# Kernel tuning notes

Measured on AMD Instinct MI355X. Metric: run time of the kernel, lower is better.

## Reference

```python
import jax, jax.numpy as jnp
import numpy as np

EMB = 300
LAYERS = 5
N_NODES = 100000
N_EDGES = 400000
N_GRAPHS = 1024
TEMP = 0.04
BN_EPS = 1e-5
SELF_LOOP_BOND_TYPE = 4  # pretrain-gnns convention: self-loop edge_attr = [4, 0]


def setup_inputs() -> dict:
    key = jax.random.key(0)
    ks = jax.random.split(key, 20)
    s = 0.02
    inp = {
        "x": jax.random.randint(ks[0], (N_NODES, 2), 0, 3, dtype=jnp.int64) if jax.config.jax_enable_x64 else jax.random.randint(ks[0], (N_NODES, 2), 0, 3, dtype=jnp.int32),
        "edge_index": jax.random.randint(ks[1], (2, N_EDGES), 0, N_NODES, dtype=jnp.int32),
        "edge_attr": jax.random.randint(ks[2], (N_EDGES, 2), 0, 3, dtype=jnp.int32),
        "batch": jnp.sort(jax.random.randint(ks[3], (N_NODES,), 0, N_GRAPHS, dtype=jnp.int32)),
        # atom embedding tables
        "atom_emb1": jax.random.normal(ks[4], (120, EMB), jnp.float32) * s,
        "atom_emb2": jax.random.normal(ks[5], (3, EMB), jnp.float32) * s,
        # per-layer bond embedding tables
        "bond_emb1": jax.random.normal(ks[6], (LAYERS, 6, EMB), jnp.float32) * s,
        "bond_emb2": jax.random.normal(ks[7], (LAYERS, 3, EMB), jnp.float32) * s,
        # per-layer GIN MLP: Linear(300,600) -> ReLU -> Linear(600,300)
        "W1": jax.random.normal(ks[8], (LAYERS, EMB, 2 * EMB), jnp.float32) * s,
        "b1": jnp.zeros((LAYERS, 2 * EMB), jnp.float32),
        "W2": jax.random.normal(ks[9], (LAYERS, 2 * EMB, EMB), jnp.float32) * s,
        "b2": jnp.zeros((LAYERS, EMB), jnp.float32),
        # per-layer batchnorm affine params
        "bn_scale": jnp.ones((LAYERS, EMB), jnp.float32),
        "bn_bias": jnp.zeros((LAYERS, EMB), jnp.float32),
        # projector: Linear(300,300) -> ReLU -> Linear(300,300)
        "pW1": jax.random.normal(ks[10], (EMB, EMB), jnp.float32) * s,
        "pb1": jnp.zeros((EMB,), jnp.float32),
        "pW2": jax.random.normal(ks[11], (EMB, EMB), jnp.float32) * s,
        "pb2": jnp.zeros((EMB,), jnp.float32),
    }
    return inp


def _forward(x, edge_index, edge_attr, batch, atom_emb1, atom_emb2, bond_emb1,
             bond_emb2, W1, b1, W2, b2, bn_scale, bn_bias, pW1, pb1, pW2, pb2):
    src, dst = edge_index[0], edge_index[1]
    h = atom_emb1[x[:, 0]] + atom_emb2[x[:, 1]]  # [N, EMB]
    for l in range(LAYERS):
        # edge embeddings for real edges + self-loop edge embedding
        e_emb = bond_emb1[l][edge_attr[:, 0]] + bond_emb2[l][edge_attr[:, 1]]  # [E, EMB]
        self_emb = bond_emb1[l][SELF_LOOP_BOND_TYPE] + bond_emb2[l][0]  # [EMB]
        # GIN sum aggregation: scatter messages + implicit self-loop message
        msg = h[src] + e_emb  # [E, EMB]
        agg = jax.ops.segment_sum(msg, dst, num_segments=N_NODES) + h + self_emb
        # MLP
        h = jax.nn.relu(agg @ W1[l] + b1[l]) @ W2[l] + b2[l]
        # batchnorm (training-mode batch statistics)
        mean = jnp.mean(h, axis=0)
        var = jnp.var(h, axis=0)
        h = (h - mean) * jax.lax.rsqrt(var + BN_EPS) * bn_scale[l] + bn_bias[l]
        if l < LAYERS - 1:
            h = jax.nn.relu(h)
    # global mean pool over graphs
    counts = jax.ops.segment_sum(jnp.ones((N_NODES,), h.dtype), batch, num_segments=N_GRAPHS)
    pooled = jax.ops.segment_sum(h, batch, num_segments=N_GRAPHS) / jnp.maximum(counts, 1.0)[:, None]
    # projector + L2 normalize
    proj = jax.nn.relu(pooled @ pW1 + pb1) @ pW2 + pb2
    norm = jnp.sqrt(jnp.sum(proj * proj, axis=1, keepdims=True))
    feats = proj / jnp.maximum(norm, 1e-12)
    f0, f1 = feats[: N_GRAPHS // 2], feats[N_GRAPHS // 2:]
    logits = (f0 @ f1.T) / TEMP  # [G/2, G/2]
    return logits


def reference(x, edge_index, edge_attr, batch, atom_emb1, atom_emb2, bond_emb1,
              bond_emb2, W1, b1, W2, b2, bn_scale, bn_bias, pW1, pb1, pW2, pb2):
    return _forward(x, edge_index, edge_attr, batch, atom_emb1, atom_emb2,
                    bond_emb1, bond_emb2, W1, b1, W2, b2, bn_scale, bn_bias,
                    pW1, pb1, pW2, pb2)
```

## Files before the change

kernel.cpp:

```cpp
#include <hip/hip_runtime.h>

#define EMB   300
#define EMB2  600
#define NLAYERS 5
#define NN    100000
#define NE    400000
#define NG    1024
#define BN_EPS 1e-5f
#define MPAD  100096
#define NB_SC 391
#define HLD   304


typedef __bf16 bf16;
typedef __attribute__((ext_vector_type(4))) __bf16 bf16x4;
typedef __attribute__((ext_vector_type(8))) __bf16 bf16x8;
typedef __attribute__((ext_vector_type(4))) float f32x4;

typedef __attribute__((address_space(3))) unsigned int lds_uint;
typedef __attribute__((address_space(1))) const unsigned int gbl_uint;

__device__ __forceinline__ void gld_lds16(const bf16* g, bf16* l) {
  __builtin_amdgcn_global_load_lds((gbl_uint*)g, (lds_uint*)l, 16, 0, 0);
}

__global__ void k_count(const int* __restrict__ dst, int* __restrict__ cnt) {
  int e = blockIdx.x * 256 + threadIdx.x;
  if (e < NE) atomicAdd(&cnt[dst[e]], 1);
}

__global__ void k_bsum(const int* __restrict__ cnt, int* __restrict__ bsum) {
  __shared__ int red[256];
  int i = blockIdx.x * 256 + threadIdx.x;
  red[threadIdx.x] = (i < NN) ? cnt[i] : 0;
  __syncthreads();
  for (int off = 128; off; off >>= 1) {
    if (threadIdx.x < off) red[threadIdx.x] += red[threadIdx.x + off];
    __syncthreads();
  }
  if (!threadIdx.x) bsum[blockIdx.x] = red[0];
}

__global__ void k_bscan(const int* __restrict__ bsum, int* __restrict__ bpre) {
  __shared__ int s[512];
  int t = threadIdx.x;
  s[t] = (t < NB_SC) ? bsum[t] : 0;
  __syncthreads();
  for (int off = 1; off < 512; off <<= 1) {
    int v = (t >= off) ? s[t - off] : 0;
    __syncthreads();
    s[t] += v;
    __syncthreads();
  }
  if (t < NB_SC) bpre[t] = t ? s[t - 1] : 0;
}

__global__ void k_expand(const int* __restrict__ cnt, const int* __restrict__ bpre,
                         int* __restrict__ rowptr, int* __restrict__ cursor) {
  __shared__ int s[256];
  int t = threadIdx.x, i = blockIdx.x * 256 + t;
  int v = (i < NN) ? cnt[i] : 0;
  s[t] = v;
  __syncthreads();
  for (int off = 1; off < 256; off <<= 1) {
    int u = (t >= off) ? s[t - off] : 0;
    __syncthreads();
    s[t] += u;
    __syncthreads();
  }
  int excl = bpre[blockIdx.x] + s[t] - v;
  if (i < NN) { rowptr[i] = excl; cursor[i] = excl; }
  if (i == NN - 1) rowptr[NN] = excl + v;
}

__global__ void k_fill(const int* __restrict__ ei, const int* __restrict__ ea,
                       int* __restrict__ cursor, int* __restrict__ packed) {
  int e = blockIdx.x * 256 + threadIdx.x;
  if (e >= NE) return;
  int d = ei[NE + e];
  int s = ei[e];
  int comb = ea[2 * e] * 3 + ea[2 * e + 1];
  int pos = atomicAdd(&cursor[d], 1);
  packed[pos] = s | (comb << 20);
}

__global__ void k_init(const int* __restrict__ x, const float4* __restrict__ ae1,
                       const float4* __restrict__ ae2, bf16* __restrict__ h) {
  int idx = blockIdx.x * 256 + threadIdx.x;
  if (idx >= NN * 76) return;
  int n = idx / 76, v = idx - n * 76;
  bf16x4 r4;
  if (v < 75) {
    int x0 = x[2 * n], x1 = x[2 * n + 1];
    float4 a = ae1[x0 * 75 + v], b = ae2[x1 * 75 + v];
    r4[0] = (bf16)(a.x + b.x); r4[1] = (bf16)(a.y + b.y);
    r4[2] = (bf16)(a.z + b.z); r4[3] = (bf16)(a.w + b.w);
  } else {
    r4[0] = r4[1] = r4[2] = r4[3] = (bf16)0.f;
  }
  *(bf16x4*)(h + (size_t)n * HLD + 4 * v) = r4;
}

__global__ void k_prepw1(const float* __restrict__ W1, bf16* __restrict__ B1n) {
  int idx = blockIdx.x * 256 + threadIdx.x;
  if (idx >= 5 * 640 * 640) return;
  int l = idx / (640 * 640), rem = idx - l * (640 * 640);
  int n = rem / 640, kp = rem - n * 640;
  int lo = kp >= 320;
  int kk = lo ? kp - 320 : kp;
  float w = (n < 600 && kk < 300) ? W1[(size_t)l * 300 * 600 + kk * 600 + n] : 0.f;
  bf16 hi = (bf16)w;
  B1n[idx] = lo ? (bf16)(w - (float)hi) : hi;
}

__global__ void k_prepw2(const float* __restrict__ W2, bf16* __restrict__ B2n) {
  int idx = blockIdx.x * 256 + threadIdx.x;
  if (idx >= 5 * 384 * 1280) return;
  int l = idx / (384 * 1280), rem = idx - l * (384 * 1280);
  int n = rem / 1280, kp = rem - n * 1280;
  int lo = kp >= 640;
  int kk = lo ? kp - 640 : kp;
  float w = (n < 300 && kk < 600) ? W2[(size_t)l * 600 * 300 + kk * 300 + n] : 0.f;
  bf16 hi = (bf16)w;
  B2n[idx] = lo ? (bf16)(w - (float)hi) : hi;
}

__global__ void k_prepb(const float* __restrict__ b1, const float* __restrict__ b2,
                        float* __restrict__ b1p, float* __restrict__ b2p) {
  int idx = blockIdx.x * 256 + threadIdx.x;
  if (idx < 5 * 640) {
    int l = idx / 640, n = idx - l * 640;
    b1p[idx] = (n < 600) ? b1[l * 600 + n] : 0.f;
  } else if (idx < 5 * 640 + 5 * 384) {
    int j = idx - 5 * 640;
    int l = j / 384, n = j - l * 384;
    b2p[j] = (n < 300) ? b2[l * 300 + n] : 0.f;
  }
}

template <int APPLY>
__global__ __launch_bounds__(256) void k_agg(
    const bf16* __restrict__ h, const int* __restrict__ rowptr,
    const int* __restrict__ packed, const float* __restrict__ be1,
    const float* __restrict__ be2, const float* __restrict__ coef,
    bf16* __restrict__ aggS) {
  __shared__ float tab[9 * HLD];
  for (int i = threadIdx.x; i < 9 * HLD; i += 256) {
    int cc = i / HLD, d = i - cc * HLD;
    tab[i] = (d < EMB)
                 ? be1[(cc / 3) * EMB + d] + be2[(cc - (cc / 3) * 3) * EMB + d]
                 : 0.f;
  }
  __syncthreads();
  const int ty = threadIdx.x >> 6, lane = threadIdx.x & 63;
  const int n = blockIdx.x * 4 + ty;
  const int c = 8 * lane;
  const bool act = lane < 38;

  float a8[8], b8[8], acc[8];
  if (act) {
#pragma unroll
    for (int j = 0; j < 8; j++) {
      int d = c + j;
      a8[j] = APPLY ? coef[d] : 1.f;
      b8[j] = APPLY ? coef[HLD + d] : 0.f;
    }
    const bf16* hn = h + (size_t)n * HLD;
#pragma unroll
    for (int j = 0; j < 8; j++) {
      int d = c + j;
      float hv = (float)hn[d];
      if (APPLY) hv = fmaxf(fmaf(a8[j], hv, b8[j]), 0.f);
      acc[j] = hv + be1[4 * EMB + d] + be2[d];
    }
  }
  int e0 = rowptr[n], e1 = rowptr[n + 1];
  for (int e = e0; e < e1; ++e) {
    int pk = packed[e];
    const bf16* hr = h + (size_t)(pk & 0xFFFFF) * HLD;
    const float* tr = tab + (pk >> 20) * HLD;
    if (act) {
      bf16x8 v = *(const bf16x8*)(hr + c);
      f32x4 t0 = *(const f32x4*)(tr + c);
      f32x4 t1 = *(const f32x4*)(tr + c + 4);
#pragma unroll
      for (int j = 0; j < 8; j++) {
        float hv = (float)v[j];
        if (APPLY) hv = fmaxf(fmaf(a8[j], hv, b8[j]), 0.f);
        acc[j] += hv + (j < 4 ? t0[j] : t1[j - 4]);
      }
    }
  }
  bf16* row = aggS + (size_t)n * 320;
  if (lane < 40) {
    bf16x8 o;
#pragma unroll
    for (int j = 0; j < 8; j++)
      o[j] = (act && c + j < EMB) ? (bf16)acc[j] : (bf16)0.f;
    *(bf16x8*)(row + c) = o;
  }
}

template <int K_SECT, int LDA, int LDB, int B_LO, int MODE, int NTILE>
__global__ __launch_bounds__(512) void k_mfma(
    const bf16* __restrict__ A,
    const bf16* __restrict__ Bn,
    const float* __restrict__ bias,
    bf16* __restrict__ C, float* __restrict__ stats, int row_limit) {
  __shared__ __align__(16) bf16 As[256 * 64];
  __shared__ __align__(16) bf16 Bs0[128 * 64];
  __shared__ __align__(16) bf16 Bs1[128 * 64];
  const int t = threadIdx.x, lane = t & 63, wid = t >> 6;
  const int wr = wid >> 1, wc = wid & 1;

  const int nwg = (int)gridDim.x;
  const int q = nwg >> 3, r = nwg & 7;
  const int xcd = blockIdx.x & 7, slot = blockIdx.x >> 3;
  const int lin = (xcd < r ? xcd * (q + 1) : r * (q + 1) + (xcd - r) * q) + slot;
  const int row0 = (lin / NTILE) * 256, n0 = (lin % NTILE) * 128;

  const int csw = (lane & 7) ^ (lane >> 3);
  const int r8  = lane >> 3;

  auto stage = [&](int kt) {
    int kbase = kt * 64;
    const bf16* ga = A  + (size_t)(row0 + wid * 32 + r8) * LDA + kbase + csw * 8;
    const bf16* gb = Bn + (size_t)(n0  + wid * 16 + r8) * LDB + kbase + csw * 8;
#pragma unroll
    for (int i = 0; i < 4; i++)
      gld_lds16(ga + (size_t)(i * 8) * LDA, &As[(wid * 32 + i * 8) * 64]);
#pragma unroll
    for (int i = 0; i < 2; i++) {
      gld_lds16(gb + (size_t)(i * 8) * LDB,        &Bs0[(wid * 16 + i * 8) * 64]);
      gld_lds16(gb + (size_t)(i * 8) * LDB + B_LO, &Bs1[(wid * 16 + i * 8) * 64]);
    }
  };

  f32x4 acc[4][4] = {};
#pragma unroll 2
  for (int kt = 0; kt < K_SECT; kt++) {
    stage(kt);
    __syncthreads();
#pragma unroll
    for (int kk = 0; kk < 2; kk++) {
      bf16x8 af[4], b0[4], b1[4];
#pragma unroll
      for (int mf = 0; mf < 4; mf++) {
        int rr = wr * 64 + mf * 16 + (lane & 15);
        int c = (kk * 4 + (lane >> 4)) ^ (rr & 7);
        af[mf] = *(const bf16x8*)((const char*)&As[0] + rr * 128 + (c << 4));
      }
#pragma unroll
      for (int nf = 0; nf < 4; nf++) {
        int n = wc * 64 + nf * 16 + (lane & 15);
        int c = (kk * 4 + (lane >> 4)) ^ (n & 7);
        b0[nf] = *(const bf16x8*)((const char*)&Bs0[0] + n * 128 + (c << 4));
        b1[nf] = *(const bf16x8*)((const char*)&Bs1[0] + n * 128 + (c << 4));
      }
#pragma unroll
      for (int mf = 0; mf < 4; mf++)
#pragma unroll
        for (int nf = 0; nf < 4; nf++) {
          acc[mf][nf] = __builtin_amdgcn_mfma_f32_16x16x32_bf16(
              af[mf], b0[nf], acc[mf][nf], 0, 0, 0);
          acc[mf][nf] = __builtin_amdgcn_mfma_f32_16x16x32_bf16(
              af[mf], b1[nf], acc[mf][nf], 0, 0, 0);
        }
    }
    __syncthreads();
  }

  const int rq = (lane >> 4) << 2;
  const int cl = lane & 15;
#pragma unroll
  for (int nf = 0; nf < 4; nf++) {
    const int gcol = n0 + wc * 64 + nf * 16 + cl;
    float s = 0.f, qq = 0.f;
#pragma unroll
    for (int mf = 0; mf < 4; mf++)
#pragma unroll
      for (int rr = 0; rr < 4; rr++) {
        int grow = row0 + wr * 64 + mf * 16 + rq + rr;
        float v = acc[mf][nf][rr] + bias[gcol];
        if (MODE == 1) {
          if (gcol < 608) C[(size_t)grow * 608 + gcol] = (bf16)fmaxf(v, 0.f);
        } else {
          if (grow < row_limit) {
            if (gcol < HLD) C[(size_t)grow * HLD + gcol] = (bf16)v;
            s += v; qq += v * v;
          }
        }
      }
    if (MODE == 2) {
      s  += __shfl_down(s, 32);  s  += __shfl_down(s, 16);
      qq += __shfl_down(qq, 32); qq += __shfl_down(qq, 16);
      if (lane < 16 && gcol < EMB) {
        atomicAdd(&stats[gcol], s);
        atomicAdd(&stats[384 + gcol], qq);
      }
    }
  }
}

__global__ void k_bnfinal(const float* __restrict__ stats, const float* __restrict__ sc,
                          const float* __restrict__ bi, float* __restrict__ coef) {
  int c = threadIdx.x;
  if (c >= HLD) return;
  if (c < EMB) {
    float mean = stats[c] * (1.0f / NN);
    float var  = stats[384 + c] * (1.0f / NN) - mean * mean;
    float inv  = rsqrtf(var + BN_EPS);
    float a = inv * sc[c];
    coef[c] = a;
    coef[HLD + c] = bi[c] - mean * a;
  } else {
    coef[c] = 0.f;
    coef[HLD + c] = 0.f;
  }
}

__device__ __forceinline__ int lowerb(const int* a, int n, int v) {
  int lo = 0, hi = n;
  while (lo < hi) { int mid = (lo + hi) >> 1; if (a[mid] < v) lo = mid + 1; else hi = mid; }
  return lo;
}

__global__ void k_pool(const bf16* __restrict__ h, const int* __restrict__ batch,
                       const float* __restrict__ coef, float* __restrict__ pooled) {
  int g = blockIdx.x;
  __shared__ int se[2];
  if (threadIdx.x == 0) { se[0] = lowerb(batch, NN, g); se[1] = lowerb(batch, NN, g + 1); }
  __syncthreads();
  int start = se[0], end = se[1];
  for (int c = threadIdx.x; c < EMB; c += 256) {
    float s = 0.f;
    for (int r = start; r < end; ++r) s += (float)h[(size_t)r * HLD + c];
    float outv = 0.f;
    if (end > start) {
      float m = s / (float)(end - start);
      outv = fmaf(coef[c], m, coef[HLD + c]);
    }
    pooled[(size_t)g * EMB + c] = outv;
  }
}

template <bool RELU>
__global__ void k_rowgemm(const float* __restrict__ X, const float* __restrict__ W,
                          const float* __restrict__ bias, float* __restrict__ Y) {
  int g = blockIdx.x;
  __shared__ float row[EMB];
  for (int i = threadIdx.x; i < EMB; i += 256) row[i] = X[(size_t)g * EMB + i];
  __syncthreads();
  for (int c = threadIdx.x; c < EMB; c += 256) {
    float acc = bias[c];
    for (int k = 0; k < EMB; k++) acc += row[k] * W[(size_t)k * EMB + c];
    if (RELU) acc = fmaxf(acc, 0.f);
    Y[(size_t)g * EMB + c] = acc;
  }
}

__global__ void k_norm(float* __restrict__ p) {
  int g = blockIdx.x;
  __shared__ float red[256];
  float s = 0.f;
  for (int c = threadIdx.x; c < EMB; c += 256) { float v = p[(size_t)g * EMB + c]; s += v * v; }
  red[threadIdx.x] = s; __syncthreads();
  for (int off = 128; off > 0; off >>= 1) {
    if (threadIdx.x < off) red[threadIdx.x] += red[threadIdx.x + off];
    __syncthreads();
  }
  float inv = 1.0f / fmaxf(sqrtf(red[0]), 1e-12f);
  for (int c = threadIdx.x; c < EMB; c += 256) p[(size_t)g * EMB + c] *= inv;
}

__global__ __launch_bounds__(256) void k_logits(const float* __restrict__ feats,
                                                float* __restrict__ out) {
  __shared__ float SA[16 * EMB];
  __shared__ float SB[16 * EMB];
  int t = threadIdx.y * 16 + threadIdx.x;
  int i0 = blockIdx.y * 16, j0 = blockIdx.x * 16;
  for (int idx = t; idx < 16 * EMB; idx += 256) {
    int r = idx / EMB, c = idx - r * EMB;
    SA[idx] = feats[(size_t)(i0 + r) * EMB + c];
    SB[idx] = feats[(size_t)(512 + j0 + r) * EMB + c];
  }
  __syncthreads();
  float acc = 0.f;
  const float* a = &SA[threadIdx.y * EMB];
  const float* b = &SB[threadIdx.x * EMB];
  for (int k = 0; k < EMB; k++) acc += a[k] * b[k];
  out[(size_t)(i0 + threadIdx.y) * 512 + j0 + threadIdx.x] = acc / 0.04f;
}

extern "C" void kernel_launch(void* const* d_in, const int* in_sizes, int n_in,
                              void* d_out, int out_size, void* d_ws, size_t ws_size,
                              hipStream_t stream) {
  const int*   x         = (const int*)d_in[0];
  const int*   ei        = (const int*)d_in[1];
  const int*   ea        = (const int*)d_in[2];
  const int*   batch     = (const int*)d_in[3];
  const float* atom_emb1 = (const float*)d_in[4];
  const float* atom_emb2 = (const float*)d_in[5];
  const float* bond_emb1 = (const float*)d_in[6];
  const float* bond_emb2 = (const float*)d_in[7];
  const float* W1        = (const float*)d_in[8];
  const float* b1        = (const float*)d_in[9];
  const float* W2        = (const float*)d_in[10];
  const float* b2        = (const float*)d_in[11];
  const float* bn_scale  = (const float*)d_in[12];
  const float* bn_bias   = (const float*)d_in[13];
  const float* pW1       = (const float*)d_in[14];
  const float* pb1       = (const float*)d_in[15];
  const float* pW2       = (const float*)d_in[16];
  const float* pb2       = (const float*)d_in[17];
  float* out = (float*)d_out;

  char* w = (char*)d_ws;
  size_t used = 0;
  auto alloc = [&](size_t bytes) {
    char* p = w + used;
    used += (bytes + 255) & ~(size_t)255;
    return p;
  };
  bf16*  h      = (bf16*)alloc((size_t)NN * HLD * 2);
  bf16*  aggS   = (bf16*)alloc((size_t)MPAD * 320 * 2);
  bf16*  B1n    = (bf16*)alloc((size_t)5 * 640 * 640 * 2);
  bf16*  B2n    = (bf16*)alloc((size_t)5 * 384 * 1280 * 2);
  float* b1p    = (float*)alloc(5 * 640 * 4);
  float* b2p    = (float*)alloc(5 * 384 * 4);
  int*   rowptr = (int*)alloc((NN + 4) * 4);
  int*   packed = (int*)alloc(NE * 4);
  float* stats  = (float*)alloc(768 * 4);
  float* coef   = (float*)alloc(2 * HLD * 4);

  int*   cnt    = (int*)aggS;
  int*   cursor = cnt + NN;
  int*   bsum   = cursor + NN;
  int*   bpre   = bsum + 512;
  float* pooled = (float*)aggS;
  float* t1     = pooled + (size_t)NG * EMB;
  float* feats  = t1 + (size_t)NG * EMB;

  long long avail = (long long)ws_size - (long long)used - 524288;
  long long rows = avail / (608 * 2);
  if (rows > MPAD) rows = MPAD;
  if (rows < 256) rows = 256;
  int nch = (int)((NN + rows - 1) / rows);
  int CHUNK = ((NN + nch - 1) / nch + 255) & ~255;
  bf16* h1S = (bf16*)(w + used);

  hipMemsetAsync(cnt, 0, NN * 4, stream);
  k_count<<<(NE + 255) / 256, 256, 0, stream>>>(ei + NE, cnt);
  k_bsum<<<NB_SC, 256, 0, stream>>>(cnt, bsum);
  k_bscan<<<1, 512, 0, stream>>>(bsum, bpre);
  k_expand<<<NB_SC, 256, 0, stream>>>(cnt, bpre, rowptr, cursor);
  k_fill<<<(NE + 255) / 256, 256, 0, stream>>>(ei, ea, cursor, packed);

  hipMemsetAsync(aggS + (size_t)NN * 320, 0, (size_t)(MPAD - NN) * 320 * 2, stream);

  k_prepw1<<<(5 * 640 * 640 + 255) / 256, 256, 0, stream>>>(W1, B1n);
  k_prepw2<<<(5 * 384 * 1280 + 255) / 256, 256, 0, stream>>>(W2, B2n);
  k_prepb<<<(5 * 640 + 5 * 384 + 255) / 256, 256, 0, stream>>>(b1, b2, b1p, b2p);

  k_init<<<(NN * 76 + 255) / 256, 256, 0, stream>>>(
      x, (const float4*)atom_emb1, (const float4*)atom_emb2, h);

  for (int l = 0; l < NLAYERS; ++l) {
    const float* be1 = bond_emb1 + (size_t)l * 6 * EMB;
    const float* be2 = bond_emb2 + (size_t)l * 3 * EMB;
    if (l == 0)
      k_agg<0><<<NN / 4, 256, 0, stream>>>(h, rowptr, packed, be1, be2, coef, aggS);
    else
      k_agg<1><<<NN / 4, 256, 0, stream>>>(h, rowptr, packed, be1, be2, coef, aggS);

    hipMemsetAsync(stats, 0, 768 * 4, stream);
    for (int c0 = 0; c0 < NN; c0 += CHUNK) {
      int m = NN - c0 < CHUNK ? NN - c0 : CHUNK;
      int mt = (m + 255) / 256;
      k_mfma<5, 320, 640, 320, 1, 5><<<5 * mt, 512, 0, stream>>>(
          aggS + (size_t)c0 * 320, B1n + (size_t)l * 640 * 640,
          b1p + l * 640, h1S, nullptr, 0);
      k_mfma<10, 608, 1280, 640, 2, 3><<<3 * mt, 512, 0, stream>>>(
          h1S, B2n + (size_t)l * 384 * 1280,
          b2p + l * 384, h + (size_t)c0 * HLD, stats, NN - c0);
    }
    k_bnfinal<<<1, 320, 0, stream>>>(stats, bn_scale + (size_t)l * EMB,
                                     bn_bias + (size_t)l * EMB, coef);
  }

  k_pool<<<NG, 256, 0, stream>>>(h, batch, coef, pooled);
  k_rowgemm<true><<<NG, 256, 0, stream>>>(pooled, pW1, pb1, t1);
  k_rowgemm<false><<<NG, 256, 0, stream>>>(t1, pW2, pb2, feats);
  k_norm<<<NG, 256, 0, stream>>>(feats);
  k_logits<<<dim3(32, 32), dim3(16, 16), 0, stream>>>(feats, out);
}
```

Baseline: 1.996 ms.

## Software-pipeline neighbor gathers and skip MFMA on padded output columns

The edge aggregation loop now prefetches the next neighbor's packed index and feature row before accumulating the current one, overlapping gather latency with arithmetic. The GEMM kernel takes a new NLIM template parameter and skips the LDS B-fragment loads and MFMAs for 16-column fragments that lie entirely beyond the real output width (608 for the first GEMM, 304 for the second). This removes wasted matrix work on padding columns. In exchange it adds per-fragment branches, which are wave-uniform, and one redundant wrap-around prefetch per node.

Result: slower. 2.263 ms (+13.4%).

```diff
diff --git a/kernel.cpp b/kernel.cpp
--- a/kernel.cpp
+++ b/kernel.cpp
@@ -175,20 +175,27 @@
     }
   }
   int e0 = rowptr[n], e1 = rowptr[n + 1];
-  for (int e = e0; e < e1; ++e) {
-    int pk = packed[e];
-    const bf16* hr = h + (size_t)(pk & 0xFFFFF) * HLD;
-    const float* tr = tab + (pk >> 20) * HLD;
-    if (act) {
-      bf16x8 v = *(const bf16x8*)(hr + c);
-      f32x4 t0 = *(const f32x4*)(tr + c);
-      f32x4 t1 = *(const f32x4*)(tr + c + 4);
-#pragma unroll
-      for (int j = 0; j < 8; j++) {
-        float hv = (float)v[j];
-        if (APPLY) hv = fmaxf(fmaf(a8[j], hv, b8[j]), 0.f);
-        acc[j] += hv + (j < 4 ? t0[j] : t1[j - 4]);
+  if (e0 < e1) {
+    int pk = packed[e0];
+    bf16x8 v;
+    if (act) v = *(const bf16x8*)(h + (size_t)(pk & 0xFFFFF) * HLD + c);
+    for (int e = e0; e < e1; ++e) {
+      int en = (e + 1 < e1) ? e + 1 : e0;
+      int pkn = packed[en];
+      bf16x8 vn;
+      if (act) vn = *(const bf16x8*)(h + (size_t)(pkn & 0xFFFFF) * HLD + c);
+      if (act) {
+        const float* tr = tab + (pk >> 20) * HLD;
+        f32x4 t0 = *(const f32x4*)(tr + c);
+        f32x4 t1 = *(const f32x4*)(tr + c + 4);
+#pragma unroll
+        for (int j = 0; j < 8; j++) {
+          float hv = (float)v[j];
+          if (APPLY) hv = fmaxf(fmaf(a8[j], hv, b8[j]), 0.f);
+          acc[j] += hv + (j < 4 ? t0[j] : t1[j - 4]);
+        }
       }
+      pk = pkn; v = vn;
     }
   }
   bf16* row = aggS + (size_t)n * 320;
@@ -201,7 +208,7 @@
   }
 }
 
-template <int K_SECT, int LDA, int LDB, int B_LO, int MODE, int NTILE>
+template <int K_SECT, int LDA, int LDB, int B_LO, int MODE, int NTILE, int NLIM>
 __global__ __launch_bounds__(512) void k_mfma(
     const bf16* __restrict__ A,
     const bf16* __restrict__ Bn,
@@ -247,24 +254,28 @@
 #pragma unroll
       for (int mf = 0; mf < 4; mf++) {
         int rr = wr * 64 + mf * 16 + (lane & 15);
-        int c = (kk * 4 + (lane >> 4)) ^ (rr & 7);
-        af[mf] = *(const bf16x8*)((const char*)&As[0] + rr * 128 + (c << 4));
+        int cc = (kk * 4 + (lane >> 4)) ^ (rr & 7);
+        af[mf] = *(const bf16x8*)((const char*)&As[0] + rr * 128 + (cc << 4));
       }
 #pragma unroll
       for (int nf = 0; nf < 4; nf++) {
-        int n = wc * 64 + nf * 16 + (lane & 15);
-        int c = (kk * 4 + (lane >> 4)) ^ (n & 7);
-        b0[nf] = *(const bf16x8*)((const char*)&Bs0[0] + n * 128 + (c << 4));
-        b1[nf] = *(const bf16x8*)((const char*)&Bs1[0] + n * 128 + (c << 4));
+        if (n0 + wc * 64 + nf * 16 < NLIM) {
+          int n = wc * 64 + nf * 16 + (lane & 15);
+          int cc = (kk * 4 + (lane >> 4)) ^ (n & 7);
+          b0[nf] = *(const bf16x8*)((const char*)&Bs0[0] + n * 128 + (cc << 4));
+          b1[nf] = *(const bf16x8*)((const char*)&Bs1[0] + n * 128 + (cc << 4));
+        }
       }
 #pragma unroll
       for (int mf = 0; mf < 4; mf++)
 #pragma unroll
         for (int nf = 0; nf < 4; nf++) {
-          acc[mf][nf] = __builtin_amdgcn_mfma_f32_16x16x32_bf16(
-              af[mf], b0[nf], acc[mf][nf], 0, 0, 0);
-          acc[mf][nf] = __builtin_amdgcn_mfma_f32_16x16x32_bf16(
-              af[mf], b1[nf], acc[mf][nf], 0, 0, 0);
+          if (n0 + wc * 64 + nf * 16 < NLIM) {
+            acc[mf][nf] = __builtin_amdgcn_mfma_f32_16x16x32_bf16(
+                af[mf], b0[nf], acc[mf][nf], 0, 0, 0);
+            acc[mf][nf] = __builtin_amdgcn_mfma_f32_16x16x32_bf16(
+                af[mf], b1[nf], acc[mf][nf], 0, 0, 0);
+          }
         }
     }
     __syncthreads();
@@ -477,10 +488,10 @@
     for (int c0 = 0; c0 < NN; c0 += CHUNK) {
       int m = NN - c0 < CHUNK ? NN - c0 : CHUNK;
       int mt = (m + 255) / 256;
-      k_mfma<5, 320, 640, 320, 1, 5><<<5 * mt, 512, 0, stream>>>(
+      k_mfma<5, 320, 640, 320, 1, 5, 608><<<5 * mt, 512, 0, stream>>>(
           aggS + (size_t)c0 * 320, B1n + (size_t)l * 640 * 640,
           b1p + l * 640, h1S, nullptr, 0);
-      k_mfma<10, 608, 1280, 640, 2, 3><<<3 * mt, 512, 0, stream>>>(
+      k_mfma<10, 608, 1280, 640, 2, 3, 304><<<3 * mt, 512, 0, stream>>>(
           h1S, B2n + (size_t)l * 384 * 1280,
           b2p + l * 384, h + (size_t)c0 * HLD, stats, NN - c0);
     }
```
